# Kernel tuning notes

Measured on AMD Instinct MI355X. Metric: run time of the kernel, lower is better.

## Reference

```python
import jax, jax.numpy as jnp
import numpy as np

PAD = 26
H = 1900
B = 256
T_EPI = 25
T_ANT = 64
T_TOT = 153
EMB = 10
IC = 2 * H  # classifier in_channels = 3800


def setup_inputs() -> dict:
    key = jax.random.key(0)
    ks = jax.random.split(key, 16)
    def rn(i, s, sc):
        return jax.random.normal(ks[i], s, jnp.float32) * sc
    inp = {
        "epitope_x": jax.random.randint(ks[0], (B, T_EPI), 0, 26),
        "left_antigen_x": jax.random.randint(ks[1], (B, T_ANT), 0, 26),
        "right_antigen_x": jax.random.randint(ks[2], (B, T_ANT), 0, 26),
        "total_antigen_x": jax.random.randint(ks[3], (B, T_TOT), 0, 26),
        "embed": rn(4, (27, EMB), 0.1),
        "wx": rn(5, (EMB, 4 * H), 0.1),
        "wh": rn(6, (H, 4 * H), 0.02),
        "wmx": rn(7, (EMB, H), 0.1),
        "wmh": rn(8, (H, H), 0.02),
        "b": rn(9, (4 * H,), 0.1),
        "gx": jnp.ones((4 * H,), jnp.float32),
        "gh": jnp.ones((4 * H,), jnp.float32),
        "gmx": jnp.ones((H,), jnp.float32),
        "gmh": jnp.ones((H,), jnp.float32),
        "bn1_gamma": jnp.ones((IC,), jnp.float32),
        "bn1_beta": jnp.zeros((IC,), jnp.float32),
        "bn1_mean": jnp.zeros((IC,), jnp.float32),
        "bn1_var": jnp.ones((IC,), jnp.float32),
        "W1": rn(10, (IC, IC // 10), 0.02),
        "b1": jnp.zeros((IC // 10,), jnp.float32),
        "bn2_gamma": jnp.ones((IC // 10,), jnp.float32),
        "bn2_beta": jnp.zeros((IC // 10,), jnp.float32),
        "bn2_mean": jnp.zeros((IC // 10,), jnp.float32),
        "bn2_var": jnp.ones((IC // 10,), jnp.float32),
        "W2": rn(11, (IC // 10, 1), 0.05),
        "b2": jnp.zeros((1,), jnp.float32),
    }
    return inp


def _wn(w, g):
    # tf.nn.l2_normalize(w, dim=0) * g  (eps 1e-12)
    return w * (g * jax.lax.rsqrt(jnp.maximum(jnp.sum(w * w, axis=0, keepdims=True), 1e-12)))


def _mlstm(xs, wx, wh, wmx, wmh, b):
    # xs: [T, B, E] -> hidden states [B, T, H]
    nB = xs.shape[1]
    def step(carry, x):
        c, h = carry
        m = (x @ wmx) * (h @ wmh)
        z = x @ wx + m @ wh + b
        i, f, o, u = jnp.split(z, 4, axis=1)
        c = jax.nn.sigmoid(f) * c + jax.nn.sigmoid(i) * jnp.tanh(u)
        h = jax.nn.sigmoid(o) * jnp.tanh(c)
        return (c, h), h
    init = (jnp.zeros((nB, H), xs.dtype), jnp.zeros((nB, H), xs.dtype))
    _, hs = jax.lax.scan(step, init, xs)
    return jnp.swapaxes(hs, 0, 1)


def _forward(epitope_x, left_antigen_x, right_antigen_x, total_antigen_x, embed,
             wx, wh, wmx, wmh, b, gx, gh, gmx, gmh,
             bn1_gamma, bn1_beta, bn1_mean, bn1_var, W1, b1,
             bn2_gamma, bn2_beta, bn2_mean, bn2_var, W2, b2):
    wxn = _wn(wx, gx); whn = _wn(wh, gh); wmxn = _wn(wmx, gmx); wmhn = _wn(wmh, gmh)
    epi_len = jnp.sum((epitope_x != PAD).astype(jnp.int32), axis=1)
    left_len = jnp.maximum(jnp.sum((left_antigen_x != PAD).astype(jnp.int32), axis=1), 1)
    right_len = jnp.maximum(jnp.sum((right_antigen_x != PAD).astype(jnp.int32), axis=1), 1)
    tot_len = epi_len + left_len + right_len
    epi_emb = embed[epitope_x]          # [B, 25, 10]
    tot_emb = embed[total_antigen_x]    # [B, 153, 10]
    epi_hs = _mlstm(jnp.swapaxes(epi_emb, 0, 1), wxn, whn, wmxn, wmhn, b)   # [B, 25, H]
    tot_hs = _mlstm(jnp.swapaxes(tot_emb, 0, 1), wxn, whn, wmxn, wmhn, b)   # [B, 153, H]
    ei = jnp.clip(epi_len - 1, 0, epi_hs.shape[1] - 1)
    ti = jnp.clip(tot_len - 1, 0, tot_hs.shape[1] - 1)
    epi_h = jnp.take_along_axis(epi_hs, ei[:, None, None], axis=1)[:, 0]
    tot_h = jnp.take_along_axis(tot_hs, ti[:, None, None], axis=1)[:, 0]
    x = jnp.concatenate([tot_h, epi_h], axis=-1)  # [B, 3800]
    lrelu = lambda v: jnp.where(v >= 0, v, 0.3 * v)
    bn = lambda v, g, bt, m, vv: (v - m) * jax.lax.rsqrt(vv + 1e-3) * g + bt
    x = bn(lrelu(x), bn1_gamma, bn1_beta, bn1_mean, bn1_var)
    x = x @ W1 + b1
    x = bn(lrelu(x), bn2_gamma, bn2_beta, bn2_mean, bn2_var)
    x = x @ W2 + b2
    return x.reshape(-1)


def reference(epitope_x, left_antigen_x, right_antigen_x, total_antigen_x, embed,
              wx, wh, wmx, wmh, b, gx, gh, gmx, gmh,
              bn1_gamma, bn1_beta, bn1_mean, bn1_var, W1, b1,
              bn2_gamma, bn2_beta, bn2_mean, bn2_var, W2, b2):
    return _forward(epitope_x, left_antigen_x, right_antigen_x, total_antigen_x, embed,
                    wx, wh, wmx, wmh, b, gx, gh, gmx, gmh,
                    bn1_gamma, bn1_beta, bn1_mean, bn1_var, W1, b1,
                    bn2_gamma, bn2_beta, bn2_mean, bn2_var, W2, b2)
```

## Files before the change

### kernel.cpp

```cpp
#include <hip/hip_runtime.h>


typedef _Float16 f16;
typedef _Float16 half8 __attribute__((ext_vector_type(8)));
typedef float f32x4 __attribute__((ext_vector_type(4)));

#define H_    1900
#define HP    1920
#define NKA   60
#define NKB   61
#define NKF   120
#define NR    512
#define TT    153
#define TE    25
#define EMB_  10
#define FCN   384

__device__ __forceinline__ float sigm(float x) {
  float p = __expf(-fabsf(x));
  float r = 1.f / (1.f + p);
  return x >= 0.f ? r : 1.f - r;
}
__device__ __forceinline__ float tanh_(float x) {
  float p = __expf(-2.f * fabsf(x));
  float r = (1.f - p) / (1.f + p);
  return x >= 0.f ? r : -r;
}

__device__ __forceinline__ void gll16(const f16* g, f16* l) {
  __builtin_amdgcn_global_load_lds(
      (const __attribute__((address_space(1))) unsigned int*)g,
      (__attribute__((address_space(3))) unsigned int*)l, 16, 0, 0);
}


__global__ void k_norms_p(const float* __restrict__ wh, const float* __restrict__ wx,
                          const float* __restrict__ wmh, const float* __restrict__ wmx,
                          float* __restrict__ part) {
  int seg = blockIdx.x & 3;
  int tid = (blockIdx.x >> 2) * 256 + threadIdx.x;
  float s = 0.f;
  if (tid < 7600) {
    int k0 = seg * 475;
    for (int k = k0; k < k0 + 475; k++) { float v = wh[(size_t)k * 7600 + tid]; s += v * v; }
  } else if (tid < 15200) {
    if (seg == 0) {
      int n = tid - 7600;
      for (int e = 0; e < EMB_; e++) { float v = wx[(size_t)e * 7600 + n]; s += v * v; }
    }
  } else if (tid < 17100) {
    int n = tid - 15200; int k0 = seg * 475;
    for (int k = k0; k < k0 + 475; k++) { float v = wmh[(size_t)k * H_ + n]; s += v * v; }
  } else if (tid < 19000) {
    if (seg == 0) {
      int n = tid - 17100;
      for (int e = 0; e < EMB_; e++) { float v = wmx[(size_t)e * H_ + n]; s += v * v; }
    }
  }
  if (tid < 19000) part[(size_t)seg * 19000 + tid] = s;
}

__global__ void k_norms_f(const float* __restrict__ part,
                          const float* __restrict__ gh, const float* __restrict__ gx,
                          const float* __restrict__ gmh, const float* __restrict__ gmx,
                          float* __restrict__ inv_wh, float* __restrict__ inv_wx,
                          float* __restrict__ inv_wmh, float* __restrict__ inv_wmx) {
  int tid = blockIdx.x * 256 + threadIdx.x;
  if (tid >= 19000) return;
  float s = part[tid] + part[19000 + tid] + part[38000 + tid] + part[57000 + tid];
  float r = rsqrtf(fmaxf(s, 1e-12f));
  if (tid < 7600)        inv_wh[tid] = gh[tid] * r;
  else if (tid < 15200)  { int n = tid - 7600;  inv_wx[n]  = gx[n]  * r; }
  else if (tid < 17100)  { int n = tid - 15200; inv_wmh[n] = gmh[n] * r; }
  else                   { int n = tid - 17100; inv_wmx[n] = gmx[n] * r; }
}

__global__ void k_wmhS(const float* __restrict__ wmh, const float* __restrict__ inv,
                       f16* __restrict__ WmhS) {
  int i = blockIdx.x * 256 + threadIdx.x;
  if (i >= 1920 * 1920) return;
  int n = i % 1920, k = i / 1920;
  float v = (n < H_ && k < H_) ? wmh[(size_t)k * H_ + n] * inv[n] : 0.f;
  int c = n >> 4, nl = n & 15, kb = k >> 5, kl = k & 31;
  WmhS[(((size_t)c * NKA + kb) * 512) + (nl + 16 * (kl >> 3)) * 8 + (kl & 7)] = (f16)v;
}

__global__ void k_whS(const float* __restrict__ wh, const float* __restrict__ wx,
                      const float* __restrict__ bias,
                      const float* __restrict__ inv_wh, const float* __restrict__ inv_wx,
                      f16* __restrict__ WhS) {
  int i = blockIdx.x * 256 + threadIdx.x;
  if (i >= 7600 * 1952) return;
  int col = i % 7600, k = i / 7600;
  float v = 0.f;
  if (k < H_)                        v = wh[(size_t)k * 7600 + col] * inv_wh[col];
  else if (k >= HP && k < HP + EMB_) v = wx[(size_t)(k - HP) * 7600 + col] * inv_wx[col];
  else if (k == HP + EMB_)           v = bias[col];
  int g = col / H_, n = col % H_;
  int q = n >> 4, nl = n & 15, kb = k >> 5, kl = k & 31;
  WhS[(((size_t)(q * 4 + g) * NKB + kb) * 512) + (nl + 16 * (kl >> 3)) * 8 + (kl & 7)] = (f16)v;
}

__global__ void k_wmxT(const float* __restrict__ wmx, const float* __restrict__ inv_wmx,
                       f16* __restrict__ wmxT) {
  int i = blockIdx.x * 256 + threadIdx.x;
  if (i >= HP * 32) return;
  int n = i >> 5, k = i & 31;
  float v = (k < EMB_ && n < H_) ? wmx[(size_t)k * H_ + n] * inv_wmx[n] : 0.f;
  wmxT[i] = (f16)v;
}

__global__ void k_lens(const int* __restrict__ ex, const int* __restrict__ lx,
                       const int* __restrict__ rx, int* __restrict__ sel) {
  int s = threadIdx.x;
  int el = 0; for (int i = 0; i < 25; i++) el += (ex[s * 25 + i] != 26);
  int ll = 0; for (int i = 0; i < 64; i++) ll += (lx[s * 64 + i] != 26);
  int rl = 0; for (int i = 0; i < 64; i++) rl += (rx[s * 64 + i] != 26);
  ll = ll < 1 ? 1 : ll;  rl = rl < 1 ? 1 : rl;
  int tl = el + ll + rl;
  int ti = tl - 1; ti = ti < 0 ? 0 : (ti > 152 ? 152 : ti);
  int ei = el - 1; ei = ei < 0 ? 0 : (ei > 24 ? 24 : ei);
  sel[s] = ti; sel[256 + s] = ei;
}

__global__ void k_init(f16* __restrict__ h0, f16* __restrict__ h1, float* __restrict__ c) {
  int i = blockIdx.x * 256 + threadIdx.x;
  if (i < NR * HP) { h0[i] = (f16)0.f; h1[i] = (f16)0.f; c[i] = 0.f; }
}

__global__ void k_xe16(const int* __restrict__ totx, const int* __restrict__ epix,
                       const float* __restrict__ embed, f16* __restrict__ xe16) {
  int i = blockIdx.x * blockDim.x + threadIdx.x;
  if (i >= TT * NR) return;
  int t = i / NR, r = i % NR;
  int tok = -1;
  if (r < 256) tok = totx[r * TT + t];
  else if (t < TE) tok = epix[(r - 256) * TE + t];
  f16* o = xe16 + (size_t)i * 32;
  #pragma unroll
  for (int e = 0; e < EMB_; e++) o[e] = (f16)(tok >= 0 ? embed[tok * EMB_ + e] : 0.f);
  o[10] = (f16)1.f;
  #pragma unroll
  for (int e = 11; e < 32; e++) o[e] = (f16)0.f;
}


__global__ __launch_bounds__(256, 2)
void k_stepA(const f16* __restrict__ hS, const f16* __restrict__ WmhS,
             const f16* __restrict__ xe16_t, const f16* __restrict__ wmxT,
             f16* __restrict__ mS, int rgc) {
  __shared__ __align__(16) f16 Bb[2][8][2][512];
  const int lane = threadIdx.x & 63, wid = threadIdx.x >> 6;
  const int bi = blockIdx.x;
  const int x = bi & 7, mm = bi >> 3;
  const int rg = mm % rgc, rem = mm / rgc;
  const int cbh = rem & 1, chi = rem >> 1;
  const int ct = chi * 8 + x;
  if (ct >= 30) return;
  const int rtile = rg * 4 + wid;
  const int r0 = rtile * 16;
  const int l16 = lane & 15, l4 = lane >> 4;

  const f16* Abase = hS   + (size_t)rtile * NKA * 512 + lane * 8;
  const f16* Bglob = WmhS + (size_t)(ct * 4 + cbh * 2) * NKA * 512 + lane * 8;

  f32x4 xm[2];
  {
    half8 xa = *(const half8*)(xe16_t + (size_t)(r0 + l16) * 32 + l4 * 8);
    #pragma unroll
    for (int cb = 0; cb < 2; cb++) {
      half8 xb = *(const half8*)(wmxT + (size_t)(ct * 64 + (cbh * 2 + cb) * 16 + l16) * 32 + l4 * 8);
      f32x4 z = {0.f, 0.f, 0.f, 0.f};
      xm[cb] = __builtin_amdgcn_mfma_f32_16x16x32_f16(xa, xb, z, 0, 0, 0);
    }
  }

  half8 Areg[2][8];
  f32x4 acc[2];
  #pragma unroll
  for (int cb = 0; cb < 2; cb++) { f32x4 z = {0.f, 0.f, 0.f, 0.f}; acc[cb] = z; }

#define STAGE_A(g, buf, n_) { _Pragma("unroll") for (int q_ = 0; q_ < ((n_) >> 1); q_++) { \
    int p_ = wid * ((n_) >> 1) + q_; int kbl_ = p_ >> 1, cb_ = p_ & 1; \
    gll16(Bglob + ((size_t)cb_ * NKA + (g) * 8 + kbl_) * 512, &Bb[buf][kbl_][cb_][0]); } }
#define LOADA_A(g, buf, n_) { _Pragma("unroll") for (int kk_ = 0; kk_ < 8; kk_++) if (kk_ < (n_)) \
    Areg[buf][kk_] = *(const half8*)(Abase + (size_t)((g) * 8 + kk_) * 512); }
#define COMP_A(g, buf, n_) { _Pragma("unroll") for (int kk_ = 0; kk_ < 8; kk_++) if (kk_ < (n_)) { \
    half8 b0_ = *(const half8*)&Bb[buf][kk_][0][lane * 8]; \
    half8 b1_ = *(const half8*)&Bb[buf][kk_][1][lane * 8]; \
    acc[0] = __builtin_amdgcn_mfma_f32_16x16x32_f16(Areg[buf][kk_], b0_, acc[0], 0, 0, 0); \
    acc[1] = __builtin_amdgcn_mfma_f32_16x16x32_f16(Areg[buf][kk_], b1_, acc[1], 0, 0, 0); } }

  LOADA_A(0, 0, 8); STAGE_A(0, 0, 8);
  __syncthreads();
  #pragma unroll
  for (int g = 0; g < 8; g++) {
    const int nn = (g == 7) ? 4 : 8;
    if (g < 7) {
      const int nn1 = (g == 6) ? 4 : 8;
      STAGE_A(g + 1, (g + 1) & 1, nn1); LOADA_A(g + 1, (g + 1) & 1, nn1);
    }
    COMP_A(g, g & 1, nn);
    __syncthreads();
  }
#undef STAGE_A
#undef LOADA_A
#undef COMP_A

  const int q4 = lane >> 4, c16 = lane & 15;
  const int kb = ct * 2 + cbh;
  #pragma unroll
  for (int cb = 0; cb < 2; cb++) {
    int klane = cb * 16 + c16;
    int lf = (klane >> 3) * 16;
    int sub = c16 & 7;
    f16* dst = mS + ((size_t)rtile * NKB + kb) * 512 + sub;
    #pragma unroll
    for (int q = 0; q < 4; q++) {
      int rl = q4 * 4 + q;
      dst[(rl + lf) * 8] = (f16)(acc[cb][q] * xm[cb][q]);
    }
  }
  if (ct == 0 && cbh == 0) {
    f16* dst = mS + ((size_t)rtile * NKB + 60) * 512 + lane * 8;
    *(half8*)dst = *(const half8*)(xe16_t + (size_t)(r0 + l16) * 32 + l4 * 8);
  }
}

__global__ __launch_bounds__(256, 1)
void k_stepB(const f16* __restrict__ mS, const f16* __restrict__ WhS,
             float* __restrict__ c, f16* __restrict__ houtS,
             float* __restrict__ selH, const int* __restrict__ sel, int t, int rgc) {
  __shared__ __align__(16) f16 Bb[2][8][4][512];
  const int lane = threadIdx.x & 63, wid = threadIdx.x >> 6;
  const int bi = blockIdx.x;
  const int x = bi & 7, mm = bi >> 3;
  const int rg = mm % rgc, chi = mm / rgc;
  const int colq = chi * 8 + x;
  if (colq >= 119) return;
  const int rt0 = (rg * 4 + wid) * 2;
  const int r0 = rt0 * 16;

  const f16* Abase = mS  + (size_t)rt0 * NKB * 512 + lane * 8;
  const f16* Bglob = WhS + (size_t)(colq * 4) * NKB * 512 + lane * 8;

  half8 Areg[2][8][2];
  f32x4 acc[2][4];
  #pragma unroll
  for (int a = 0; a < 2; a++)
    #pragma unroll
    for (int b = 0; b < 4; b++) { f32x4 z = {0.f, 0.f, 0.f, 0.f}; acc[a][b] = z; }

#define STAGE_B(g, buf, n_) { _Pragma("unroll") for (int q_ = 0; q_ < 8; q_++) { \
    int p_ = wid * 8 + q_; \
    if (p_ < (n_) * 4) { int kbl_ = p_ >> 2, gg_ = p_ & 3; \
      gll16(Bglob + ((size_t)gg_ * NKB + (g) * 8 + kbl_) * 512, &Bb[buf][kbl_][gg_][0]); } } }
#define LOADA_B(g, buf, n_) { _Pragma("unroll") for (int kk_ = 0; kk_ < 8; kk_++) if (kk_ < (n_)) { \
    Areg[buf][kk_][0] = *(const half8*)(Abase + (size_t)((g) * 8 + kk_) * 512); \
    Areg[buf][kk_][1] = *(const half8*)(Abase + ((size_t)NKB + (g) * 8 + kk_) * 512); } }
#define COMP_B(g, buf, n_) { _Pragma("unroll") for (int kk_ = 0; kk_ < 8; kk_++) if (kk_ < (n_)) { \
    half8 b0_ = *(const half8*)&Bb[buf][kk_][0][lane * 8]; \
    half8 b1_ = *(const half8*)&Bb[buf][kk_][1][lane * 8]; \
    half8 b2_ = *(const half8*)&Bb[buf][kk_][2][lane * 8]; \
    half8 b3_ = *(const half8*)&Bb[buf][kk_][3][lane * 8]; \
    _Pragma("unroll") for (int rf_ = 0; rf_ < 2; rf_++) { \
      acc[rf_][0] = __builtin_amdgcn_mfma_f32_16x16x32_f16(Areg[buf][kk_][rf_], b0_, acc[rf_][0], 0, 0, 0); \
      acc[rf_][1] = __builtin_amdgcn_mfma_f32_16x16x32_f16(Areg[buf][kk_][rf_], b1_, acc[rf_][1], 0, 0, 0); \
      acc[rf_][2] = __builtin_amdgcn_mfma_f32_16x16x32_f16(Areg[buf][kk_][rf_], b2_, acc[rf_][2], 0, 0, 0); \
      acc[rf_][3] = __builtin_amdgcn_mfma_f32_16x16x32_f16(Areg[buf][kk_][rf_], b3_, acc[rf_][3], 0, 0, 0); } } }

  LOADA_B(0, 0, 8); STAGE_B(0, 0, 8);
  __syncthreads();
  #pragma unroll
  for (int g = 0; g < 8; g++) {
    const int nn = (g == 7) ? 5 : 8;
    if (g < 7) {
      const int nn1 = (g == 6) ? 5 : 8;
      STAGE_B(g + 1, (g + 1) & 1, nn1); LOADA_B(g + 1, (g + 1) & 1, nn1);
    }
    COMP_B(g, g & 1, nn);
    __syncthreads();
  }
#undef STAGE_B
#undef LOADA_B
#undef COMP_B

  const int q4 = lane >> 4, c16 = lane & 15;
  const int j = colq * 16 + c16;
  const bool valid = j < H_;
  const int kbh = colq >> 1;
  const int lfh = ((((colq & 1) * 16 + c16) >> 3)) * 16;
  const int subh = c16 & 7;
  #pragma unroll
  for (int rf = 0; rf < 2; rf++) {
    f16* hdst = houtS + ((size_t)(rt0 + rf) * NKA + kbh) * 512 + subh;
    #pragma unroll
    for (int q = 0; q < 4; q++) {
      int rl = q4 * 4 + q;
      int row = r0 + rf * 16 + rl;
      if (valid) {
        size_t idx = (size_t)row * HP + j;
        float cold = c[idx];
        float iz = acc[rf][0][q], fz = acc[rf][1][q];
        float oz = acc[rf][2][q], uz = acc[rf][3][q];
        float cn = sigm(fz) * cold + sigm(iz) * tanh_(uz);
        float hv = sigm(oz) * tanh_(cn);
        c[idx] = cn;
        hdst[(rl + lfh) * 8] = (f16)hv;
        if (t == sel[row]) selH[idx] = hv;
      }
    }
  }
}


__global__ void k_xqS(const float* __restrict__ selH, const float* __restrict__ g1,
                      const float* __restrict__ be1, const float* __restrict__ mu1,
                      const float* __restrict__ var1, f16* __restrict__ xqS) {
  int i = blockIdx.x * 256 + threadIdx.x;
  if (i >= 256 * 3840) return;
  int k = i % 3840, s = i / 3840;
  float v = 0.f; bool have = false;
  if (k < H_)            { v = selH[(size_t)s * HP + k]; have = true; }
  else if (k < 2 * H_)   { v = selH[(size_t)(256 + s) * HP + (k - H_)]; have = true; }
  float q = 0.f;
  if (have) {
    float lr = v < 0.f ? 0.3f * v : v;
    q = (lr - mu1[k]) * rsqrtf(var1[k] + 1e-3f) * g1[k] + be1[k];
  }
  int rtile = s >> 4, sl = s & 15, kb = k >> 5, kl = k & 31;
  xqS[(((size_t)rtile * NKF + kb) * 512) + (sl + 16 * (kl >> 3)) * 8 + (kl & 7)] = (f16)q;
}

__global__ void k_w1S(const float* __restrict__ W1, f16* __restrict__ W1S) {
  int i = blockIdx.x * 256 + threadIdx.x;
  if (i >= 384 * 3840) return;
  int col = i % 384, k = i / 384;
  float v = (col < 380 && k < 2 * H_) ? W1[(size_t)k * 380 + col] : 0.f;
  int cg = col >> 4, nl = col & 15, kb = k >> 5, kl = k & 31;
  W1S[(((size_t)cg * NKF + kb) * 512) + (nl + 16 * (kl >> 3)) * 8 + (kl & 7)] = (f16)v;
}

__global__ __launch_bounds__(256)
void k_fc1(const f16* __restrict__ xqS, const f16* __restrict__ W1S,
           const float* __restrict__ b1, float* __restrict__ z1) {
  const int lane = threadIdx.x & 63, wid = threadIdx.x >> 6;
  const int ct = blockIdx.x % 6, rg = blockIdx.x / 6;
  const int rtile = rg * 4 + wid;
  const int r0 = rtile * 16;

  const f16* Abase = xqS + (size_t)rtile * NKF * 512 + lane * 8;
  const f16* Bbase = W1S + (size_t)(ct * 4) * NKF * 512 + lane * 8;

  half8 fa0, fa1, fa2, fa3;
  half8 fb0[4], fb1[4], fb2[4], fb3[4];
  f32x4 acc[4];
  #pragma unroll
  for (int cb = 0; cb < 4; cb++) { f32x4 z = {0.f, 0.f, 0.f, 0.f}; acc[cb] = z; }

#define LDA_F(d, kb)  d = *(const half8*)(Abase + (size_t)(kb) * 512)
#define LDB_F(d, kb)  { _Pragma("unroll") for (int cb = 0; cb < 4; cb++) \
    d[cb] = *(const half8*)(Bbase + ((size_t)cb * NKF + (kb)) * 512); }
#define MMA_F(fa, fb) { _Pragma("unroll") for (int cb = 0; cb < 4; cb++) \
    acc[cb] = __builtin_amdgcn_mfma_f32_16x16x32_f16(fa, fb[cb], acc[cb], 0, 0, 0); }

  LDA_F(fa0, 0); LDB_F(fb0, 0);
  LDA_F(fa1, 1); LDB_F(fb1, 1);
  LDA_F(fa2, 2); LDB_F(fb2, 2);
  for (int base = 0; base < 116; base += 4) {
    LDA_F(fa3, base + 3); LDB_F(fb3, base + 3);
    MMA_F(fa0, fb0);
    LDA_F(fa0, base + 4); LDB_F(fb0, base + 4);
    MMA_F(fa1, fb1);
    LDA_F(fa1, base + 5); LDB_F(fb1, base + 5);
    MMA_F(fa2, fb2);
    LDA_F(fa2, base + 6); LDB_F(fb2, base + 6);
    MMA_F(fa3, fb3);
  }
  LDA_F(fa3, 119); LDB_F(fb3, 119);
  MMA_F(fa0, fb0);
  MMA_F(fa1, fb1);
  MMA_F(fa2, fb2);
  MMA_F(fa3, fb3);
#undef LDA_F
#undef LDB_F
#undef MMA_F

  const int q4 = lane >> 4, c16 = lane & 15;
  #pragma unroll
  for (int cb = 0; cb < 4; cb++)
    #pragma unroll
    for (int q = 0; q < 4; q++) {
      int row = r0 + q4 * 4 + q;
      int col = ct * 64 + cb * 16 + c16;
      float bias = (col < 380) ? b1[col] : 0.f;
      z1[(size_t)row * FCN + col] = acc[cb][q] + bias;
    }
}

__global__ void k_fc2(const float* __restrict__ z1, const float* __restrict__ g2,
                      const float* __restrict__ be2, const float* __restrict__ mu2,
                      const float* __restrict__ var2, const float* __restrict__ W2,
                      const float* __restrict__ b2, float* __restrict__ out) {
  int s = threadIdx.x;
  float a = 0.f;
  for (int jj = 0; jj < 380; jj++) {
    float v = z1[(size_t)s * FCN + jj];
    float lr = v < 0.f ? 0.3f * v : v;
    float q = (lr - mu2[jj]) * rsqrtf(var2[jj] + 1e-3f) * g2[jj] + be2[jj];
    a += q * W2[jj];
  }
  out[s] = a + b2[0];
}


extern "C" void kernel_launch(void* const* d_in, const int* in_sizes, int n_in,
                              void* d_out, int out_size, void* d_ws, size_t ws_size,
                              hipStream_t stream) {
  const int*   epix  = (const int*)d_in[0];
  const int*   lx    = (const int*)d_in[1];
  const int*   rx    = (const int*)d_in[2];
  const int*   totx  = (const int*)d_in[3];
  const float* embed = (const float*)d_in[4];
  const float* wx    = (const float*)d_in[5];
  const float* wh    = (const float*)d_in[6];
  const float* wmx   = (const float*)d_in[7];
  const float* wmh   = (const float*)d_in[8];
  const float* bb    = (const float*)d_in[9];
  const float* gx    = (const float*)d_in[10];
  const float* gh    = (const float*)d_in[11];
  const float* gmx   = (const float*)d_in[12];
  const float* gmh   = (const float*)d_in[13];
  const float* bn1g  = (const float*)d_in[14];
  const float* bn1b  = (const float*)d_in[15];
  const float* bn1m  = (const float*)d_in[16];
  const float* bn1v  = (const float*)d_in[17];
  const float* W1    = (const float*)d_in[18];
  const float* b1    = (const float*)d_in[19];
  const float* bn2g  = (const float*)d_in[20];
  const float* bn2b  = (const float*)d_in[21];
  const float* bn2m  = (const float*)d_in[22];
  const float* bn2v  = (const float*)d_in[23];
  const float* W2    = (const float*)d_in[24];
  const float* b2v   = (const float*)d_in[25];

  char* base = (char*)d_ws;
  size_t off = 0;
  auto alloc = [&](size_t n) { char* p = base + off; off = (off + n + 255) & ~(size_t)255; return p; };

  f16*   WmhS   = (f16*)  alloc((size_t)120 * NKA * 512 * 2);
  f16*   WhS    = (f16*)  alloc((size_t)119 * 4 * NKB * 512 * 2);
  f16*   wmxT   = (f16*)  alloc((size_t)HP * 32 * 2);
  f16*   xe16   = (f16*)  alloc((size_t)TT * NR * 32 * 2);
  f16*   h0S    = (f16*)  alloc((size_t)32 * NKA * 512 * 2);
  f16*   h1S    = (f16*)  alloc((size_t)32 * NKA * 512 * 2);
  f16*   mS     = (f16*)  alloc((size_t)32 * NKB * 512 * 2);
  float* cst    = (float*)alloc((size_t)NR * HP * 4);
  float* selH   = (float*)alloc((size_t)NR * HP * 4);
  int*   sel    = (int*)  alloc((size_t)NR * 4);
  float* inv_wh = (float*)alloc(7600 * 4);
  float* inv_wx = (float*)alloc(7600 * 4);
  float* inv_wmh= (float*)alloc(1900 * 4);
  float* inv_wmx= (float*)alloc(1900 * 4);
  float* npart  = (float*)alloc((size_t)4 * 19000 * 4);
  f16*   xqS    = (f16*)  alloc((size_t)16 * NKF * 512 * 2);
  f16*   W1S    = (f16*)  alloc((size_t)24 * NKF * 512 * 2);
  float* z1     = (float*)alloc((size_t)256 * FCN * 4);
  (void)in_sizes; (void)n_in; (void)out_size; (void)ws_size;

  hipLaunchKernelGGL(k_norms_p, dim3(300), dim3(256), 0, stream, wh, wx, wmh, wmx, npart);
  hipLaunchKernelGGL(k_norms_f, dim3(75), dim3(256), 0, stream,
                     npart, gh, gx, gmh, gmx, inv_wh, inv_wx, inv_wmh, inv_wmx);
  hipLaunchKernelGGL(k_wmhS, dim3((1920 * 1920 + 255) / 256), dim3(256), 0, stream,
                     wmh, inv_wmh, WmhS);
  hipLaunchKernelGGL(k_whS, dim3((7600 * 1952 + 255) / 256), dim3(256), 0, stream,
                     wh, wx, bb, inv_wh, inv_wx, WhS);
  hipLaunchKernelGGL(k_wmxT, dim3((HP * 32 + 255) / 256), dim3(256), 0, stream,
                     wmx, inv_wmx, wmxT);
  hipLaunchKernelGGL(k_lens, dim3(1), dim3(256), 0, stream, epix, lx, rx, sel);
  hipLaunchKernelGGL(k_init, dim3((NR * HP + 255) / 256), dim3(256), 0, stream,
                     h0S, h1S, cst);
  hipLaunchKernelGGL(k_xe16, dim3((TT * NR + 255) / 256), dim3(256), 0, stream,
                     totx, epix, embed, xe16);

  for (int t = 0; t < TT; t++) {
    int Mt = (t < TE) ? NR : 256;
    const f16* hin = (t & 1) ? h1S : h0S;
    f16*       ho  = (t & 1) ? h0S : h1S;
    int rgcA = Mt / 64;
    int rgcB = Mt / 128;
    hipLaunchKernelGGL(k_stepA, dim3(64 * rgcA), dim3(256), 0, stream,
                       hin, WmhS, xe16 + (size_t)t * NR * 32, wmxT, mS, rgcA);
    hipLaunchKernelGGL(k_stepB, dim3(8 * rgcB * 15), dim3(256), 0, stream,
                       mS, WhS, cst, ho, selH, sel, t, rgcB);
  }

  hipLaunchKernelGGL(k_xqS, dim3((256 * 3840 + 255) / 256), dim3(256), 0, stream,
                     selH, bn1g, bn1b, bn1m, bn1v, xqS);
  hipLaunchKernelGGL(k_w1S, dim3((384 * 3840 + 255) / 256), dim3(256), 0, stream, W1, W1S);
  hipLaunchKernelGGL(k_fc1, dim3(24), dim3(256), 0, stream, xqS, W1S, b1, z1);
  hipLaunchKernelGGL(k_fc2, dim3(1), dim3(256), 0, stream,
                     z1, bn2g, bn2b, bn2m, bn2v, W2, b2v, (float*)d_out);
}
```

Baseline: 4.694 ms.

## Halve k_stepB per-wave row tiles and k-group to double block count

Each wave in k_stepB now computes one 16-row tile instead of two. The k loop is split into 16 groups of 4 k-blocks instead of 8 groups of 8, which halves the LDS staging buffer and register arrays. Launch bounds allow 2 blocks per CU, and the grid doubles via rgcB = Mt/64, so more CUs and waves are busy during the latency-bound recurrent step. The cost is half the reuse of each staged Wh tile, so Wh is re-read from L2 or cache twice as often, and there are more __syncthreads barriers per block.

```diff
diff --git a/kernel.cpp b/kernel.cpp
--- a/kernel.cpp
+++ b/kernel.cpp
@@ -227,55 +227,50 @@
   }
 }
 
-__global__ __launch_bounds__(256, 1)
+__global__ __launch_bounds__(256, 2)
 void k_stepB(const f16* __restrict__ mS, const f16* __restrict__ WhS,
              float* __restrict__ c, f16* __restrict__ houtS,
              float* __restrict__ selH, const int* __restrict__ sel, int t, int rgc) {
-  __shared__ __align__(16) f16 Bb[2][8][4][512];
+  __shared__ __align__(16) f16 Bb[2][4][4][512];
   const int lane = threadIdx.x & 63, wid = threadIdx.x >> 6;
   const int bi = blockIdx.x;
   const int x = bi & 7, mm = bi >> 3;
   const int rg = mm % rgc, chi = mm / rgc;
   const int colq = chi * 8 + x;
   if (colq >= 119) return;
-  const int rt0 = (rg * 4 + wid) * 2;
-  const int r0 = rt0 * 16;
-
-  const f16* Abase = mS  + (size_t)rt0 * NKB * 512 + lane * 8;
+  const int rtile = rg * 4 + wid;
+  const int r0 = rtile * 16;
+
+  const f16* Abase = mS  + (size_t)rtile * NKB * 512 + lane * 8;
   const f16* Bglob = WhS + (size_t)(colq * 4) * NKB * 512 + lane * 8;
 
-  half8 Areg[2][8][2];
-  f32x4 acc[2][4];
-  #pragma unroll
-  for (int a = 0; a < 2; a++)
-    #pragma unroll
-    for (int b = 0; b < 4; b++) { f32x4 z = {0.f, 0.f, 0.f, 0.f}; acc[a][b] = z; }
-
-#define STAGE_B(g, buf, n_) { _Pragma("unroll") for (int q_ = 0; q_ < 8; q_++) { \
-    int p_ = wid * 8 + q_; \
-    if (p_ < (n_) * 4) { int kbl_ = p_ >> 2, gg_ = p_ & 3; \
-      gll16(Bglob + ((size_t)gg_ * NKB + (g) * 8 + kbl_) * 512, &Bb[buf][kbl_][gg_][0]); } } }
-#define LOADA_B(g, buf, n_) { _Pragma("unroll") for (int kk_ = 0; kk_ < 8; kk_++) if (kk_ < (n_)) { \
-    Areg[buf][kk_][0] = *(const half8*)(Abase + (size_t)((g) * 8 + kk_) * 512); \
-    Areg[buf][kk_][1] = *(const half8*)(Abase + ((size_t)NKB + (g) * 8 + kk_) * 512); } }
-#define COMP_B(g, buf, n_) { _Pragma("unroll") for (int kk_ = 0; kk_ < 8; kk_++) if (kk_ < (n_)) { \
+  half8 Areg[2][4];
+  f32x4 acc[4];
+  #pragma unroll
+  for (int b = 0; b < 4; b++) { f32x4 z = {0.f, 0.f, 0.f, 0.f}; acc[b] = z; }
+
+#define STAGE_B(g, buf, n_) { _Pragma("unroll") for (int q_ = 0; q_ < (n_); q_++) { \
+    int p_ = wid * (n_) + q_; int kbl_ = p_ >> 2, gg_ = p_ & 3; \
+    gll16(Bglob + ((size_t)gg_ * NKB + (g) * 4 + kbl_) * 512, &Bb[buf][kbl_][gg_][0]); } }
+#define LOADA_B(g, buf, n_) { _Pragma("unroll") for (int kk_ = 0; kk_ < 4; kk_++) if (kk_ < (n_)) \
+    Areg[buf][kk_] = *(const half8*)(Abase + (size_t)((g) * 4 + kk_) * 512); }
+#define COMP_B(g, buf, n_) { _Pragma("unroll") for (int kk_ = 0; kk_ < 4; kk_++) if (kk_ < (n_)) { \
     half8 b0_ = *(const half8*)&Bb[buf][kk_][0][lane * 8]; \
     half8 b1_ = *(const half8*)&Bb[buf][kk_][1][lane * 8]; \
     half8 b2_ = *(const half8*)&Bb[buf][kk_][2][lane * 8]; \
     half8 b3_ = *(const half8*)&Bb[buf][kk_][3][lane * 8]; \
-    _Pragma("unroll") for (int rf_ = 0; rf_ < 2; rf_++) { \
-      acc[rf_][0] = __builtin_amdgcn_mfma_f32_16x16x32_f16(Areg[buf][kk_][rf_], b0_, acc[rf_][0], 0, 0, 0); \
-      acc[rf_][1] = __builtin_amdgcn_mfma_f32_16x16x32_f16(Areg[buf][kk_][rf_], b1_, acc[rf_][1], 0, 0, 0); \
-      acc[rf_][2] = __builtin_amdgcn_mfma_f32_16x16x32_f16(Areg[buf][kk_][rf_], b2_, acc[rf_][2], 0, 0, 0); \
-      acc[rf_][3] = __builtin_amdgcn_mfma_f32_16x16x32_f16(Areg[buf][kk_][rf_], b3_, acc[rf_][3], 0, 0, 0); } } }
-
-  LOADA_B(0, 0, 8); STAGE_B(0, 0, 8);
+    acc[0] = __builtin_amdgcn_mfma_f32_16x16x32_f16(Areg[buf][kk_], b0_, acc[0], 0, 0, 0); \
+    acc[1] = __builtin_amdgcn_mfma_f32_16x16x32_f16(Areg[buf][kk_], b1_, acc[1], 0, 0, 0); \
+    acc[2] = __builtin_amdgcn_mfma_f32_16x16x32_f16(Areg[buf][kk_], b2_, acc[2], 0, 0, 0); \
+    acc[3] = __builtin_amdgcn_mfma_f32_16x16x32_f16(Areg[buf][kk_], b3_, acc[3], 0, 0, 0); } }
+
+  LOADA_B(0, 0, 4); STAGE_B(0, 0, 4);
   __syncthreads();
   #pragma unroll
-  for (int g = 0; g < 8; g++) {
-    const int nn = (g == 7) ? 5 : 8;
-    if (g < 7) {
-      const int nn1 = (g == 6) ? 5 : 8;
+  for (int g = 0; g < 16; g++) {
+    const int nn = (g == 15) ? 1 : 4;
+    if (g < 15) {
+      const int nn1 = (g == 14) ? 1 : 4;
       STAGE_B(g + 1, (g + 1) & 1, nn1); LOADA_B(g + 1, (g + 1) & 1, nn1);
     }
     COMP_B(g, g & 1, nn);
@@ -291,24 +286,21 @@
   const int kbh = colq >> 1;
   const int lfh = ((((colq & 1) * 16 + c16) >> 3)) * 16;
   const int subh = c16 & 7;
-  #pragma unroll
-  for (int rf = 0; rf < 2; rf++) {
-    f16* hdst = houtS + ((size_t)(rt0 + rf) * NKA + kbh) * 512 + subh;
-    #pragma unroll
-    for (int q = 0; q < 4; q++) {
-      int rl = q4 * 4 + q;
-      int row = r0 + rf * 16 + rl;
-      if (valid) {
-        size_t idx = (size_t)row * HP + j;
-        float cold = c[idx];
-        float iz = acc[rf][0][q], fz = acc[rf][1][q];
-        float oz = acc[rf][2][q], uz = acc[rf][3][q];
-        float cn = sigm(fz) * cold + sigm(iz) * tanh_(uz);
-        float hv = sigm(oz) * tanh_(cn);
-        c[idx] = cn;
-        hdst[(rl + lfh) * 8] = (f16)hv;
-        if (t == sel[row]) selH[idx] = hv;
-      }
+  f16* hdst = houtS + ((size_t)rtile * NKA + kbh) * 512 + subh;
+  #pragma unroll
+  for (int q = 0; q < 4; q++) {
+    int rl = q4 * 4 + q;
+    int row = r0 + rl;
+    if (valid) {
+      size_t idx = (size_t)row * HP + j;
+      float cold = c[idx];
+      float iz = acc[0][q], fz = acc[1][q];
+      float oz = acc[2][q], uz = acc[3][q];
+      float cn = sigm(fz) * cold + sigm(iz) * tanh_(uz);
+      float hv = sigm(oz) * tanh_(cn);
+      c[idx] = cn;
+      hdst[(rl + lfh) * 8] = (f16)hv;
+      if (t == sel[row]) selH[idx] = hv;
     }
   }
 }
@@ -488,7 +480,7 @@
     const f16* hin = (t & 1) ? h1S : h0S;
     f16*       ho  = (t & 1) ? h0S : h1S;
     int rgcA = Mt / 64;
-    int rgcB = Mt / 128;
+    int rgcB = Mt / 64;
     hipLaunchKernelGGL(k_stepA, dim3(64 * rgcA), dim3(256), 0, stream,
                        hin, WmhS, xe16 + (size_t)t * NR * 32, wmxT, mS, rgcA);
     hipLaunchKernelGGL(k_stepB, dim3(8 * rgcB * 15), dim3(256), 0, stream,
```

New measurement: 4.308 ms. -8.2%, faster.
